# Optimization experiments

Measured on AMD Instinct MI355X. Metric: run time of the kernel, lower is better.

Reference implementation:

```python
import jax, jax.numpy as jnp
import numpy as np

DIM = 128
HEADS = 8
DK = DIM // HEADS
HID = DIM * 4
# torch: scores / math.sqrt(scale) with scale = 1/dim**0.5  ->  multiply by dim**0.25
INV = float(1.0 / np.sqrt(1.0 / np.sqrt(DIM)))


def _ln(x, g, b, eps=1e-5):
    m = jnp.mean(x, axis=-1, keepdims=True)
    v = jnp.mean((x - m) ** 2, axis=-1, keepdims=True)
    return (x - m) / jnp.sqrt(v + eps) * g + b


def _lin(x, w, b):  # torch Linear: x @ W.T + b, W:[out,in]
    return jnp.einsum('...i,oi->...o', x, w) + b


def _attention_new(node, edge, w, bv):
    # node [b,n,c], edge [b,n,n,c]; raw torch .view => row-major reshape
    b, n, c = node.shape
    q = _lin(node, w[0], bv[0]).reshape(b, HEADS, n, DK)
    k = _lin(edge, w[1], bv[1]).reshape(b, HEADS, n, n, DK)
    v = _lin(node, w[2], bv[2]).reshape(b, HEADS, n, DK)
    s = jnp.einsum('bhmd,bhmnd->bhmn', q, k) * INV
    out_attn = jax.nn.softmax(s, axis=-1)
    in_attn = jax.nn.softmax(jnp.swapaxes(s, -1, -2), axis=-1)
    eye = jnp.eye(n, dtype=s.dtype)
    # out_attn + in_attn - diag_embed(diagonal(out_attn))
    message = out_attn + in_attn - eye * out_attn
    node_h = jnp.einsum('bhmn,bhnd->bhmd', message, v).reshape(b, n, c)
    edge_h = jnp.einsum('bhmn,bhand->bhamd', message, k).reshape(b, n, n, c)
    return _lin(node_h, w[4], bv[4]), _lin(edge_h, w[3], bv[3]), message


def _enc_dec_attention(mx, px, ma, pa, w, bv):
    b, n, c = mx.shape
    P = px.shape[1]
    qx = _lin(mx, w[0], bv[0]).reshape(b, HEADS, n, DK)
    kx = _lin(px, w[1], bv[1]).reshape(b, HEADS, P, DK)
    vx = _lin(mx, w[2], bv[2]).reshape(b, HEADS, n, DK)
    qa = _lin(ma, w[3], bv[3]).reshape(b, HEADS, n, n, DK)
    ka = _lin(pa, w[4], bv[4]).reshape(b, HEADS, P, P, DK)
    va = _lin(ma, w[5], bv[5]).reshape(b, HEADS, n, n, DK)
    s = jnp.einsum('bhmd,bhnd->bhmn', qx, kx) * INV  # [b,h,n,P]
    out_attn = jax.nn.softmax(s, axis=-1)
    in_attn = jax.nn.softmax(jnp.swapaxes(s, -1, -2), axis=-1)
    message = out_attn + jnp.swapaxes(in_attn, -1, -2)
    # einsum 'bhmn,bhmd->bhmd': sum over n, elementwise scale of v
    node_h = jnp.sum(message, axis=-1)[..., None] * vx
    # 'bhmnd,bhkjd->bhmn': contract d after summing key over (k,j)
    ksum = jnp.sum(ka, axis=(2, 3))  # [b,h,d]
    se = jnp.einsum('bhmnd,bhd->bhmn', qa, ksum) * INV
    oa = jax.nn.softmax(se, axis=-1)
    ia = jax.nn.softmax(jnp.swapaxes(se, -1, -2), axis=-1)
    me = oa + jnp.swapaxes(ia, -1, -2)
    # 'bhmn,bhmkd->bhmnd': contract k
    edge_h = me[..., None] * jnp.sum(va, axis=3)[:, :, :, None, :]
    node_h = _lin(node_h.reshape(b, n, c), w[6], bv[6])
    edge_h = _lin(edge_h.reshape(b, n, n, c), w[7], bv[7])
    return edge_h, node_h, message


def _mlp(x, w1, b1, w2, b2):
    return _lin(jax.nn.sigmoid(_lin(x, w1, b1)), w2, b2)


def _decoder_block(mol_annot, prot_annot, mol_adj, prot_adj,
                   att_w, att_b, dec_w, dec_b,
                   mlp_w1, mlp_b1, mlp_w2, mlp_b2, ln_g, ln_b):
    mx = _ln(mol_annot, ln_g[2], ln_b[2])
    px = _ln(prot_annot, ln_g[3], ln_b[3])
    ma = _ln(mol_adj, ln_g[0], ln_b[0])
    pa = _ln(prot_adj, ln_g[1], ln_b[1])
    px1, pa1, _ = _attention_new(px, pa, att_w, att_b)
    px1 = _ln(px + px1, ln_g[5], ln_b[5])
    pa1 = _ln(pa + pa1, ln_g[4], ln_b[4])
    ma1, mx1, attn_dec = _enc_dec_attention(mx, px1, ma, pa1, dec_w, dec_b)
    ma1 = _ln(ma + ma1, ln_g[6], ln_b[6])
    mx1 = _ln(mx + mx1, ln_g[7], ln_b[7])
    ma2 = _mlp(ma1, mlp_w1[0], mlp_b1[0], mlp_w2[0], mlp_b2[0]) + ma1
    mx2 = _mlp(mx1, mlp_w1[1], mlp_b1[1], mlp_w2[1], mlp_b2[1]) + mx1
    edge_hidden = _ln(ma2, ln_g[8], ln_b[8])
    node_hidden = _ln(mx2, ln_g[9], ln_b[9])
    return edge_hidden, node_hidden, attn_dec


def setup_inputs() -> dict:
    key = jax.random.key(0)
    ks = jax.random.split(key, 16)
    B, N, P = 8, 64, 256
    inp = {
        'mol_annot': jax.random.normal(ks[0], (B, N, DIM), jnp.float32),
        'prot_annot': jax.random.normal(ks[1], (B, P, DIM), jnp.float32),
        'mol_adj': jax.random.normal(ks[2], (B, N, N, DIM), jnp.float32),
        'prot_adj': jax.random.normal(ks[3], (B, P, P, DIM), jnp.float32),
        # Attention_new linears: [q,k,v,out_e,out_n]
        'att_w': jax.random.normal(ks[4], (5, DIM, DIM), jnp.float32) * 0.02,
        'att_b': jax.random.normal(ks[5], (5, DIM), jnp.float32) * 0.02,
        # enc_dec linears: [q_mx,k_px,v_mx,q_ma,k_pa,v_ma,out_mx,out_ma]
        'dec_w': jax.random.normal(ks[6], (8, DIM, DIM), jnp.float32) * 0.02,
        'dec_b': jax.random.normal(ks[7], (8, DIM), jnp.float32) * 0.02,
        # MLPs: index 0 = mlp_ma, 1 = mlp_mx
        'mlp_w1': jax.random.normal(ks[8], (2, HID, DIM), jnp.float32) * 0.02,
        'mlp_b1': jax.random.normal(ks[9], (2, HID), jnp.float32) * 0.02,
        'mlp_w2': jax.random.normal(ks[10], (2, DIM, HID), jnp.float32) * 0.02,
        'mlp_b2': jax.random.normal(ks[11], (2, DIM), jnp.float32) * 0.02,
        # LayerNorms: [ln1_ma,ln1_pa,ln1_mx,ln1_px,ln2_pa,ln2_px,ln3_ma,ln3_mx,ln4_ma,ln4_mx]
        'ln_g': jnp.ones((10, DIM), jnp.float32),
        'ln_b': jnp.zeros((10, DIM), jnp.float32),
    }
    return inp


def reference(mol_annot, prot_annot, mol_adj, prot_adj, att_w, att_b,
              dec_w, dec_b, mlp_w1, mlp_b1, mlp_w2, mlp_b2, ln_g, ln_b):
    return _decoder_block(mol_annot, prot_annot, mol_adj, prot_adj,
                          att_w, att_b, dec_w, dec_b,
                          mlp_w1, mlp_b1, mlp_w2, mlp_b2, ln_g, ln_b)
```

## Files before the change

kernel.cpp:

```cpp
#include <hip/hip_runtime.h>
#include <hip/hip_bf16.h>
#include <math.h>

#define INV_SCALE 3.3635856610148585f

typedef float f32x4 __attribute__((ext_vector_type(4)));
typedef short bf16x8 __attribute__((ext_vector_type(8)));
typedef unsigned short u16;
#define MFMA(a_, b_, c_) __builtin_amdgcn_mfma_f32_16x16x32_bf16(a_, b_, c_, 0, 0, 0)

constexpr int WT_ATT = 0;
constexpr int WT_DEC = 81920;
constexpr int WT_M1  = 212992;
constexpr int WT_M2  = 344064;
constexpr int O_PX   = 475136;
constexpr int O_MX   = 737280;
constexpr int O_MA   = 802816;
constexpr int O_QL   = 4997120;
constexpr int O_VL   = 5259264;
constexpr int O_QXL  = 5521408;
constexpr int O_VXL  = 5586944;
constexpr int O_KXL  = 5652480;
constexpr int O_PX1  = 5914624;
constexpr int O_MX1  = 6176768;
constexpr int O_S    = 6242304;
constexpr int O_MSG  = 10469376;
constexpr int O_NH   = 14663680;
constexpr int O_RS   = 14925824;
constexpr int O_KS   = 14934016;
constexpr int O_SE   = 14935040;
constexpr int O_ME2  = 15197184;
constexpr int O_VAS  = 15459328;
constexpr int O_MROW = 15524864;
constexpr int O_S2   = 15528960;
constexpr int O_MA1  = 16577536;

constexpr int OUT1_OFF = 4194304;
constexpr int OUT2_OFF = 4259840;

__device__ __forceinline__ float waveSum(float v) {
#pragma unroll
  for (int o = 32; o > 0; o >>= 1) v += __shfl_down(v, o, 64);
  return v;
}

__device__ __forceinline__ void split1(float a, u16& h, u16& l) {
  unsigned ua = __float_as_uint(a) & 0xffff0000u;
  h = (u16)(ua >> 16);
  float al = a - __uint_as_float(ua);
  l = (u16)(__float_as_uint(al) >> 16);
}
__device__ __forceinline__ void split8(const float* p, bf16x8& hi, bf16x8& lo) {
#pragma unroll
  for (int i = 0; i < 8; i++) {
    float a = p[i];
    unsigned ua = __float_as_uint(a) & 0xffff0000u;
    float al = a - __uint_as_float(ua);
    hi[i] = (short)(u16)(ua >> 16);
    lo[i] = (short)(u16)(__float_as_uint(al) >> 16);
  }
}
__device__ __forceinline__ u16 rne1(float a) {
  unsigned u = __float_as_uint(a);
  u += 0x7fffu + ((u >> 16) & 1u);
  return (u16)(u >> 16);
}
__device__ __forceinline__ bf16x8 rne8(const float* p) {
  bf16x8 h;
#pragma unroll
  for (int i = 0; i < 8; i++) h[i] = (short)rne1(p[i]);
  return h;
}

__global__ __launch_bounds__(256) void prep_wt(
    const float* __restrict__ att_w, const float* __restrict__ dec_w,
    const float* __restrict__ mlp_w1, const float* __restrict__ mlp_w2,
    float* __restrict__ ws) {
  int seg = blockIdx.x, t = threadIdx.x;
  if (seg < 5) {
    const float* w = att_w + seg * 16384;
    if (seg == 1 || seg == 3) {
      u16* oh = (u16*)(ws + WT_ATT + seg * 16384);
      for (int idx = t; idx < 16384; idx += 256) {
        int e = idx & 7, lane = (idx >> 3) & 63, kk = (idx >> 9) & 3, q = idx >> 11;
        int o = q * 16 + (lane & 15), i = kk * 32 + (lane >> 4) * 8 + e;
        u16 hh, ll; split1(w[o * 128 + i], hh, ll);
        oh[idx] = hh; oh[16384 + idx] = ll;
      }
    } else {
      float* o = ws + WT_ATT + seg * 16384;
      for (int idx = t; idx < 16384; idx += 256) o[idx] = w[(idx & 127) * 128 + (idx >> 7)];
    }
  } else if (seg < 13) {
    int k = seg - 5;
    const float* w = dec_w + k * 16384;
    float* o = ws + WT_DEC + k * 16384;
    for (int idx = t; idx < 16384; idx += 256) o[idx] = w[(idx & 127) * 128 + (idx >> 7)];
  } else if (seg < 15) {
    int k = seg - 13;
    const float* w = mlp_w1 + k * 65536;
    u16* oh = (u16*)(ws + WT_M1 + k * 65536);
    for (int idx = t; idx < 65536; idx += 256) {
      int e = idx & 7, lane = (idx >> 3) & 63, kk = (idx >> 9) & 3, q = idx >> 11;
      int o = q * 16 + (lane & 15), i = kk * 32 + (lane >> 4) * 8 + e;
      oh[idx] = rne1(w[o * 128 + i]); oh[65536 + idx] = 0;
    }
  } else {
    int k = seg - 15;
    const float* w = mlp_w2 + k * 65536;
    u16* oh = (u16*)(ws + WT_M2 + k * 65536);
    for (int idx = t; idx < 65536; idx += 256) {
      int e = idx & 7, lane = (idx >> 3) & 63, kk = (idx >> 9) & 15, q = idx >> 13;
      int o = q * 16 + (lane & 15), i = kk * 32 + (lane >> 4) * 8 + e;
      oh[idx] = rne1(w[o * 512 + i]); oh[65536 + idx] = 0;
    }
  }
}

__global__ __launch_bounds__(128) void ln_rows4(const float* __restrict__ in, float* __restrict__ out,
                                                const float* __restrict__ g, const float* __restrict__ b) {
  int t = threadIdx.x;
  size_t row = (size_t)blockIdx.x * 4 + (t >> 5);
  int c4 = (t & 31) * 4;
  float4 x = *(const float4*)&in[row * 128 + c4];
  float s = x.x + x.y + x.z + x.w;
#pragma unroll
  for (int o = 16; o > 0; o >>= 1) s += __shfl_xor(s, o, 64);
  float mean = s * (1.f / 128.f);
  float dx = x.x - mean, dy = x.y - mean, dz = x.z - mean, dw = x.w - mean;
  float v = dx * dx + dy * dy + dz * dz + dw * dw;
#pragma unroll
  for (int o = 16; o > 0; o >>= 1) v += __shfl_xor(v, o, 64);
  float rstd = rsqrtf(v * (1.f / 128.f) + 1e-5f);
  float4 gv = *(const float4*)&g[c4];
  float4 bv = *(const float4*)&b[c4];
  float4 o4;
  o4.x = dx * rstd * gv.x + bv.x;
  o4.y = dy * rstd * gv.y + bv.y;
  o4.z = dz * rstd * gv.z + bv.z;
  o4.w = dw * rstd * gv.w + bv.w;
  *(float4*)&out[row * 128 + c4] = o4;
}

__global__ __launch_bounds__(128) void lin_rows2(const float* __restrict__ in,
                                                 float* __restrict__ out1, const float* __restrict__ WT1,
                                                 const float* __restrict__ b1v,
                                                 float* __restrict__ out2, const float* __restrict__ WT2,
                                                 const float* __restrict__ b2v) {
  int row = blockIdx.x, t = threadIdx.x;
  __shared__ float rl[128];
  rl[t] = in[(size_t)row * 128 + t];
  __syncthreads();
  float a1 = b1v[t], a2 = b2v[t];
#pragma unroll 8
  for (int i = 0; i < 128; i++) {
    float rv = rl[i];
    a1 += rv * WT1[i * 128 + t];
    a2 += rv * WT2[i * 128 + t];
  }
  out1[(size_t)row * 128 + t] = a1;
  out2[(size_t)row * 128 + t] = a2;
}

__global__ __launch_bounds__(128) void lin_rows(const float* __restrict__ in, float* __restrict__ out,
                                                const float* __restrict__ WT, const float* __restrict__ bias) {
  int row = blockIdx.x, t = threadIdx.x;
  __shared__ float rl[128];
  rl[t] = in[(size_t)row * 128 + t];
  __syncthreads();
  float acc = bias[t];
#pragma unroll 8
  for (int i = 0; i < 128; i++) acc += rl[i] * WT[i * 128 + t];
  out[(size_t)row * 128 + t] = acc;
}

__device__ __forceinline__ void ln32_stats(float (*tile)[132], float* psum, float* meanL, float* rstdL,
                                           int t) {
  int r = t >> 3, seg = t & 7;
  float p = 0;
#pragma unroll
  for (int k = 0; k < 16; k++) p += tile[r][seg * 16 + k];
  psum[r * 8 + seg] = p;
  __syncthreads();
  if (t < 32) { float sm = 0; for (int k = 0; k < 8; k++) sm += psum[t * 8 + k]; meanL[t] = sm * (1.f / 128.f); }
  __syncthreads();
  float mu = meanL[r];
  p = 0;
#pragma unroll
  for (int k = 0; k < 16; k++) { float d = tile[r][seg * 16 + k] - mu; p += d * d; }
  psum[r * 8 + seg] = p;
  __syncthreads();
  if (t < 32) { float sm = 0; for (int k = 0; k < 8; k++) sm += psum[t * 8 + k]; rstdL[t] = rsqrtf(sm * (1.f / 128.f) + 1e-5f); }
  __syncthreads();
}

__device__ __forceinline__ void ln64_stats(float (*tile)[132], float* psum, float* meanL, float* rstdL,
                                           int t) {
  int r = t >> 3, seg = t & 7;
  float p = 0;
#pragma unroll
  for (int k = 0; k < 16; k++) p += tile[r][seg * 16 + k];
  psum[r * 8 + seg] = p;
  __syncthreads();
  if (t < 64) { float sm = 0; for (int k = 0; k < 8; k++) sm += psum[t * 8 + k]; meanL[t] = sm * (1.f / 128.f); }
  __syncthreads();
  float mu = meanL[r];
  p = 0;
#pragma unroll
  for (int k = 0; k < 16; k++) { float d = tile[r][seg * 16 + k] - mu; p += d * d; }
  psum[r * 8 + seg] = p;
  __syncthreads();
  if (t < 64) { float sm = 0; for (int k = 0; k < 8; k++) sm += psum[t * 8 + k]; rstdL[t] = rsqrtf(sm * (1.f / 128.f) + 1e-5f); }
  __syncthreads();
}

__global__ __launch_bounds__(256, 8) void k1_fold(
    const float* __restrict__ prot_adj, const float* __restrict__ q_lin,
    const float* __restrict__ wk_orig,
    const float* __restrict__ bk,
    const float* __restrict__ g1, const float* __restrict__ b1,
    float* __restrict__ sdst) {
  __shared__ __align__(16) float paF[32][132];
  __shared__ float wq[8][132];
  __shared__ float qL[16];
  __shared__ float psum[256];
  __shared__ float meanL[32], rstdL[32];
  int t = threadIdx.x, bid = blockIdx.x;
  int b = bid >> 11, h = (bid >> 8) & 7, ai = bid & 255;
  int irow = h * 32 + (ai >> 3), j0 = (ai & 7) * 32;
  int mq = (ai >> 3) * 8 + (ai & 7);
  size_t pabase = (((size_t)(b * 256) + irow) * 256 + j0) * 128;
  {
    const float4* src4 = (const float4*)(prot_adj + pabase);
    for (int idx = t; idx < 1024; idx += 256)
      *(float4*)&paF[idx >> 5][(idx & 31) * 4] = src4[idx];
  }
  if (t < 16) qL[t] = q_lin[((size_t)(b * 256) + h * 32 + (mq >> 3)) * 128 + (mq & 7) * 16 + t];
  __syncthreads();
#pragma unroll
  for (int k = 0; k < 4; k++) {
    int o = t + k * 256;
    int g8 = o >> 7, c = o & 127;
    float s = 0;
#pragma unroll
    for (int d = 0; d < 16; d++) s += qL[d] * wk_orig[(g8 * 16 + d) * 128 + c];
    wq[g8][c] = s;
  }
  ln32_stats(paF, psum, meanL, rstdL, t);
  for (int idx = t; idx < 4096; idx += 256) {
    int r = idx >> 7, c = idx & 127;
    paF[r][c] = (paF[r][c] - meanL[r]) * rstdL[r] * g1[c] + b1[c];
  }
  __syncthreads();
  int r = t >> 3, g8 = t & 7;
  float acc = 0;
#pragma unroll
  for (int d = 0; d < 16; d++) acc += qL[d] * bk[g8 * 16 + d];
#pragma unroll 8
  for (int c = 0; c < 128; c++) acc += paF[r][c] * wq[g8][c];
  size_t sb = ((size_t)((b * 8 + h) * 256 + mq)) * 256;
  sdst[sb + t] = INV_SCALE * acc;
}

__global__ __launch_bounds__(256) void col_part(const float* __restrict__ s, float* __restrict__ pmax,
                                                float* __restrict__ psumv) {
  int bid = blockIdx.x, t = threadIdx.x;
  int bh = bid >> 3, ch = bid & 7;
  const float* sp = s + ((size_t)(bh * 256) + ch * 32) * 256 + t;
  float rm = -3.4e38f, rs = 0.f;
  for (int r = 0; r < 32; r++) {
    float x = sp[(size_t)r * 256];
    float nm = fmaxf(rm, x);
    rs = rs * __expf(rm - nm) + __expf(x - nm);
    rm = nm;
  }
  pmax[(bh * 8 + ch) * 256 + t] = rm;
  psumv[(bh * 8 + ch) * 256 + t] = rs;
}

__global__ __launch_bounds__(256, 1) void msg_tiles(const float* __restrict__ s,
                                                    const float* __restrict__ pmax, const float* __restrict__ psumv,
                                                    const float* __restrict__ v_lin,
                                                    u16* __restrict__ mhi, u16* __restrict__ mlo,
                                                    float* __restrict__ nh) {
  __shared__ __align__(16) float rowT[32][260];
  __shared__ float sT[256][33];
  __shared__ __align__(16) u16 vTh[16][264];
  __shared__ __align__(16) u16 vTl[16][264];
  __shared__ float red[256];
  __shared__ float rmax[32], rsinv[32], cmaxL[32], csinvL[32];
  int bid = blockIdx.x, t = threadIdx.x;
  int bh = bid >> 3, m0 = (bid & 7) * 32;
  int b = bh >> 3, h = bh & 7;
  size_t sbase = (size_t)(bh * 256) * 256;
  for (int idx = t; idx < 2048; idx += 256) {
    int r = idx >> 6, c4 = (idx & 63) * 4;
    *(float4*)&rowT[r][c4] = *(const float4*)&s[sbase + (size_t)(m0 + r) * 256 + c4];
  }
  for (int idx = t; idx < 2048; idx += 256) {
    int n = idx >> 3, mc4 = (idx & 7) * 4;
    float4 v4 = *(const float4*)&s[sbase + (size_t)n * 256 + m0 + mc4];
    sT[n][mc4] = v4.x; sT[n][mc4 + 1] = v4.y; sT[n][mc4 + 2] = v4.z; sT[n][mc4 + 3] = v4.w;
  }
  {
    const float4* vb4 = (const float4*)(v_lin + ((size_t)(b * 256) + h * 32) * 128);
    for (int idx = t; idx < 1024; idx += 256) {
      float4 v4 = vb4[idx];
#pragma unroll
      for (int i = 0; i < 4; i++) {
        int flat = idx * 4 + i;
        int d = flat & 15, n = flat >> 4;
        u16 hh2, ll2; split1(((const float*)&v4)[i], hh2, ll2);
        vTh[d][n] = hh2; vTl[d][n] = ll2;
      }
    }
  }
  __syncthreads();
  {
    int r = t >> 3, sg = t & 7;
    float pm = -3.4e38f;
    for (int k = 0; k < 32; k++) pm = fmaxf(pm, rowT[r][sg * 32 + k]);
    red[t] = pm;
    __syncthreads();
    if (t < 32) { float mm = red[t * 8]; for (int k = 1; k < 8; k++) mm = fmaxf(mm, red[t * 8 + k]); rmax[t] = mm; }
    __syncthreads();
    float mm = rmax[r], ps = 0;
    for (int k = 0; k < 32; k++) ps += __expf(rowT[r][sg * 32 + k] - mm);
    red[t] = ps;
    __syncthreads();
    if (t < 32) { float sm = 0; for (int k = 0; k < 8; k++) sm += red[t * 8 + k]; rsinv[t] = 1.f / sm; }
    if (t >= 64 && t < 96) {
      int mc = t - 64, col = m0 + mc;
      float cm = -3.4e38f;
      for (int c2 = 0; c2 < 8; c2++) cm = fmaxf(cm, pmax[(bh * 8 + c2) * 256 + col]);
      float cs = 0;
      for (int c2 = 0; c2 < 8; c2++) cs += psumv[(bh * 8 + c2) * 256 + col] * __expf(pmax[(bh * 8 + c2) * 256 + col] - cm);
      cmaxL[mc] = cm; csinvL[mc] = 1.f / cs;
    }
    __syncthreads();
  }
  for (int idx = t; idx < 8192; idx += 256) {
    int r = idx >> 8, n = idx & 255;
    float x = rowT[r][n];
    float outv = __expf(x - rmax[r]) * rsinv[r];
    float inval = __expf(sT[n][r] - cmaxL[r]) * csinvL[r];
    rowT[r][n] = (n == m0 + r) ? inval : (outv + inval);
  }
  __syncthreads();
  for (int fi = t; fi < 1024; fi += 256) {
    int r = fi >> 5, fc = fi & 31;
    int m = m0 + r;
    int lane = (fc & 3) * 16 + (m & 15);
    size_t base = (size_t)bh * 65536 + (size_t)(m >> 4) * 4096 + (size_t)(fc >> 2) * 512 + lane * 8;
    bf16x8 h8, l8;
    split8(&rowT[r][fc * 8], h8, l8);
    *(bf16x8*)&mhi[base] = h8;
    *(bf16x8*)&mlo[base] = l8;
  }
  int w = t >> 6, l = t & 63, lr = l & 15, lk = l >> 4;
  if (w < 2) {
    f32x4 acc = (f32x4){0.f, 0.f, 0.f, 0.f};
#pragma unroll
    for (int kk = 0; kk < 8; kk++) {
      bf16x8 ah, al;
      split8(&rowT[w * 16 + lr][kk * 32 + lk * 8], ah, al);
      bf16x8 bhv = *(const bf16x8*)&vTh[lr][kk * 32 + lk * 8];
      bf16x8 blv = *(const bf16x8*)&vTl[lr][kk * 32 + lk * 8];
      acc = MFMA(ah, bhv, acc);
      acc = MFMA(al, bhv, acc);
      acc = MFMA(ah, blv, acc);
    }
#pragma unroll
    for (int j = 0; j < 4; j++)
      nh[((size_t)(bh * 256) + m0 + w * 16 + lk * 4 + j) * 16 + lr] = acc[j];
  }
}

__global__ __launch_bounds__(128) void px1_kernel(const float* __restrict__ px, const float* __restrict__ nh,
                                                  const float* __restrict__ WT, const float* __restrict__ bias,
                                                  const float* __restrict__ g, const float* __restrict__ bt,
                                                  float* __restrict__ px1) {
  int p = blockIdx.x, t = threadIdx.x;
  int b = p >> 8, pl = p & 255, h = pl >> 5;
  __shared__ float nodeL[128];
  __shared__ float scr[2];
  nodeL[t] = nh[((size_t)(b * 8 + h) * 256 + ((pl & 31) * 8 + (t >> 4))) * 16 + (t & 15)];
  __syncthreads();
  float acc = bias[t];
#pragma unroll 8
  for (int i = 0; i < 128; i++) acc += nodeL[i] * WT[i * 128 + t];
  float val = px[(size_t)p * 128 + t] + acc;
  float v = waveSum(val);
  if ((t & 63) == 0) scr[t >> 6] = v;
  __syncthreads();
  float mean = (scr[0] + scr[1]) * (1.f / 128.f);
  __syncthreads();
  float dd = val - mean;
  v = waveSum(dd * dd);
  if ((t & 63) == 0) scr[t >> 6] = v;
  __syncthreads();
  float rstd = rsqrtf((scr[0] + scr[1]) * (1.f / 128.f) + 1e-5f);
  px1[(size_t)p * 128 + t] = dd * rstd * g[t] + bt[t];
}

__global__ __launch_bounds__(512, 1) void s2_fused(const float* __restrict__ qxl, const float* __restrict__ kxl,
                                                   float* __restrict__ out2, float* __restrict__ mrow) {
  __shared__ float kxL[256 * 17];
  __shared__ float qxL[64 * 17];
  __shared__ float sL[64][257];
  __shared__ float rmaxL[64], rsinv[64];
  __shared__ float cmaxL[256], csinv[256];
  int bh = blockIdx.x, t = threadIdx.x;
  int b = bh >> 3, h = bh & 7;
  for (int idx = t; idx < 4096; idx += 512) {
    int pl = idx >> 7, cc = idx & 127;
    kxL[(pl * 8 + (cc >> 4)) * 17 + (cc & 15)] = kxl[((size_t)(b * 256) + h * 32 + pl) * 128 + cc];
  }
  for (int idx = t; idx < 1024; idx += 512) {
    int rl = idx >> 7, cc = idx & 127;
    qxL[(rl * 8 + (cc >> 4)) * 17 + (cc & 15)] = qxl[((size_t)(b * 64) + h * 8 + rl) * 128 + cc];
  }
  __syncthreads();
  {
    int p = t & 255, mh = t >> 8;
    float kr[16];
#pragma unroll
    for (int d = 0; d < 16; d++) kr[d] = kxL[p * 17 + d];
    for (int m = mh * 32; m < mh * 32 + 32; m++) {
      float dot = 0;
#pragma unroll
      for (int d = 0; d < 16; d++) dot += qxL[m * 17 + d] * kr[d];
      sL[m][p] = INV_SCALE * dot;
    }
  }
  __syncthreads();
  if (t < 64) {
    float mx = -3.4e38f;
    for (int p = 0; p < 256; p++) mx = fmaxf(mx, sL[t][p]);
    float sm = 0;
    for (int p = 0; p < 256; p++) sm += __expf(sL[t][p] - mx);
    rmaxL[t] = mx; rsinv[t] = 1.f / sm;
  }
  if (t < 256) {
    float mx = -3.4e38f;
    for (int m = 0; m < 64; m++) mx = fmaxf(mx, sL[m][t]);
    float sm = 0;
    for (int m = 0; m < 64; m++) sm += __expf(sL[m][t] - mx);
    cmaxL[t] = mx; csinv[t] = 1.f / sm;
  }
  __syncthreads();
  for (int idx = t; idx < 16384; idx += 512) {
    int m = idx >> 8, p = idx & 255;
    float x = sL[m][p];
    float val = __expf(x - rmaxL[m]) * rsinv[m] + __expf(x - cmaxL[p]) * csinv[p];
    out2[(size_t)bh * 16384 + idx] = val;
    sL[m][p] = val;
  }
  __syncthreads();
  if (t < 64) {
    float sm = 0;
    for (int p = 0; p < 256; p++) sm += sL[t][p];
    mrow[bh * 64 + t] = sm;
  }
}

__global__ __launch_bounds__(128) void mx1_kernel(const float* __restrict__ mx, const float* __restrict__ mrow,
                                                  const float* __restrict__ vxl, const float* __restrict__ WT,
                                                  const float* __restrict__ bias, const float* __restrict__ g,
                                                  const float* __restrict__ bt, float* __restrict__ mx1) {
  int rg = blockIdx.x, t = threadIdx.x;
  int b = rg >> 6, rl = rg & 63, h = rl >> 3;
  __shared__ float nodeL[128];
  __shared__ float scr[2];
  int m = (rl & 7) * 8 + (t >> 4);
  float vxv = vxl[((size_t)(b * 64) + h * 8 + (m >> 3)) * 128 + (m & 7) * 16 + (t & 15)];
  nodeL[t] = mrow[(b * 8 + h) * 64 + m] * vxv;
  __syncthreads();
  float acc = bias[t];
#pragma unroll 8
  for (int i = 0; i < 128; i++) acc += nodeL[i] * WT[i * 128 + t];
  float val = mx[(size_t)rg * 128 + t] + acc;
  float v = waveSum(val);
  if ((t & 63) == 0) scr[t >> 6] = v;
  __syncthreads();
  float mean = (scr[0] + scr[1]) * (1.f / 128.f);
  __syncthreads();
  float dd = val - mean;
  v = waveSum(dd * dd);
  if ((t & 63) == 0) scr[t >> 6] = v;
  __syncthreads();
  float rstd = rsqrtf((scr[0] + scr[1]) * (1.f / 128.f) + 1e-5f);
  mx1[(size_t)rg * 128 + t] = dd * rstd * g[t] + bt[t];
}

__global__ __launch_bounds__(512, 4) void k5_row(
    const float* __restrict__ prot_adj,
    const u16* __restrict__ msg_hi, const u16* __restrict__ msg_lo,
    const u16* __restrict__ wk_hi,
    const u16* __restrict__ wo_hi,
    const float* __restrict__ bk, const float* __restrict__ bo,
    const float* __restrict__ g1, const float* __restrict__ b1,
    const float* __restrict__ g4, const float* __restrict__ b4,
    float* __restrict__ rs128) {
  __shared__ __align__(16) unsigned char Lmem[72704];
  float (*paF)[132] = (float(*)[132])Lmem;
  u16* kBh = (u16*)(Lmem + 33792);
  u16* kBl = (u16*)(Lmem + 33792 + 16896);
  float (*e2)[132] = (float(*)[132])(Lmem + 33792);
  float* psum  = (float*)(Lmem + 67584);
  float* meanL = (float*)(Lmem + 69632);
  float* rstdL = (float*)(Lmem + 69888);
  float* accL  = (float*)(Lmem + 70144);
  float* scr2  = (float*)(Lmem + 70656);
  int t = threadIdx.x;
  int bid = (blockIdx.x & 7) * 256 + (blockIdx.x >> 3);
  int b = bid >> 8, h = (bid >> 5) & 7, irow_rel = bid & 31;
  int irow = h * 32 + irow_rel;
  int w = t >> 6, l = t & 63;
  const int lr = l & 15, lk = l >> 4;
  const int wr = w & 3, wq = w >> 2;
  const size_t mb = ((size_t)(b * 8 + h)) << 16;
  if (t < 128) accL[t] = 0.f;
  for (int chunk = 0; chunk < 4; chunk++) {
    __syncthreads();
    {
      size_t pabase = (((size_t)(b * 256) + irow) * 256 + chunk * 64) * 128;
      const float4* src4 = (const float4*)(prot_adj + pabase);
      for (int idx = t; idx < 2048; idx += 512)
        *(float4*)&paF[idx >> 5][(idx & 31) * 4] = src4[idx];
    }
    __syncthreads();
    ln64_stats(paF, psum, meanL, rstdL, t);
    for (int idx = t; idx < 8192; idx += 512) {
      int r = idx >> 7, c = idx & 127;
      paF[r][c] = (paF[r][c] - meanL[r]) * rstdL[r] * g1[c] + b1[c];
    }
    __syncthreads();
    {
      f32x4 acc1[4];
#pragma unroll
      for (int qq = 0; qq < 4; qq++) acc1[qq] = (f32x4){0.f, 0.f, 0.f, 0.f};
#pragma unroll 1
      for (int kk = 0; kk < 4; kk++) {
        bf16x8 ah, al;
        split8(&paF[wr * 16 + lr][kk * 32 + lk * 8], ah, al);
#pragma unroll
        for (int qq = 0; qq < 4; qq++) {
          int q = wq * 4 + qq;
          bf16x8 bh = *(const bf16x8*)&wk_hi[q * 2048 + kk * 512 + l * 8];
          bf16x8 bl = *(const bf16x8*)&wk_hi[16384 + q * 2048 + kk * 512 + l * 8];
          acc1[qq] = MFMA(ah, bh, acc1[qq]);
          acc1[qq] = MFMA(al, bh, acc1[qq]);
          acc1[qq] = MFMA(ah, bl, acc1[qq]);
        }
      }
#pragma unroll
      for (int qq = 0; qq < 4; qq++) {
        int q = wq * 4 + qq;
        float bkv = bk[q * 16 + lr];
#pragma unroll
        for (int j = 0; j < 4; j++) {
          int rloc = wr * 16 + lk * 4 + j;
          int n = (rloc & 31) * 8 + q;
          int colB = (rloc >> 5) * 16 + lr;
          u16 hh, ll; split1(acc1[qq][j] + bkv, hh, ll);
          kBh[colB * 264 + n] = hh; kBl[colB * 264 + n] = ll;
        }
      }
    }
    __syncthreads();
    f32x4 eacc[2][2];
#pragma unroll
    for (int mt = 0; mt < 2; mt++)
#pragma unroll
      for (int ct = 0; ct < 2; ct++) eacc[mt][ct] = (f32x4){0.f, 0.f, 0.f, 0.f};
#pragma unroll 1
    for (int kk = 0; kk < 8; kk++) {
      bf16x8 bhv[2], blv[2];
#pragma unroll
      for (int ct = 0; ct < 2; ct++) {
        bhv[ct] = *(const bf16x8*)&kBh[(ct * 16 + lr) * 264 + kk * 32 + lk * 8];
        blv[ct] = *(const bf16x8*)&kBl[(ct * 16 + lr) * 264 + kk * 32 + lk * 8];
      }
#pragma unroll
      for (int mt = 0; mt < 2; mt++) {
        size_t ro = mb + (size_t)((w * 2 + mt) * 4096 + kk * 512 + l * 8);
        bf16x8 ah = *(const bf16x8*)&msg_hi[ro];
        bf16x8 al = *(const bf16x8*)&msg_lo[ro];
#pragma unroll
        for (int ct = 0; ct < 2; ct++) {
          eacc[mt][ct] = MFMA(ah, bhv[ct], eacc[mt][ct]);
          eacc[mt][ct] = MFMA(al, bhv[ct], eacc[mt][ct]);
          eacc[mt][ct] = MFMA(ah, blv[ct], eacc[mt][ct]);
        }
      }
    }
    __syncthreads();
#pragma unroll
    for (int mt = 0; mt < 2; mt++)
#pragma unroll
      for (int ct = 0; ct < 2; ct++)
#pragma unroll
        for (int j = 0; j < 4; j++) {
          int m = w * 32 + mt * 16 + lk * 4 + j;
          int colE = ct * 16 + lr;
          e2[(colE >> 4) * 32 + (m >> 3)][(m & 7) * 16 + (colE & 15)] = eacc[mt][ct][j];
        }
    __syncthreads();
    {
      f32x4 oacc[4];
#pragma unroll
      for (int qq = 0; qq < 4; qq++) oacc[qq] = (f32x4){0.f, 0.f, 0.f, 0.f};
#pragma unroll 1
      for (int kk = 0; kk < 4; kk++) {
        bf16x8 ah, al;
        split8(&e2[wr * 16 + lr][kk * 32 + lk * 8], ah, al);
#pragma unroll
        for (int qq = 0; qq < 4; qq++) {
          int q = wq * 4 + qq;
          bf16x8 bh = *(const bf16x8*)&wo_hi[q * 2048 + kk * 512 + l * 8];
          bf16x8 bl = *(const bf16x8*)&wo_hi[16384 + q * 2048 + kk * 512 + l * 8];
          oacc[qq] = MFMA(ah, bh, oacc[qq]);
          oacc[qq] = MFMA(al, bh, oacc[qq]);
          oacc[qq] = MFMA(ah, bl, oacc[qq]);
        }
      }
      __syncthreads();
#pragma unroll
      for (int qq = 0; qq < 4; qq++) {
        int o = (wq * 4 + qq) * 16 + lr;
        float bv = bo[o];
#pragma unroll
        for (int j = 0; j < 4; j++) {
          int rloc = wr * 16 + lk * 4 + j;
          paF[rloc][o] = oacc[qq][j] + bv + paF[rloc][o];
        }
      }
    }
    __syncthreads();
    ln64_stats(paF, psum, meanL, rstdL, t);
    {
      int c = t & 127, rh = t >> 7;
      float part = 0;
#pragma unroll
      for (int rr = 0; rr < 16; rr++) {
        int r2 = rh * 16 + rr;
        part += (paF[r2][c] - meanL[r2]) * rstdL[r2];
      }
      scr2[rh * 128 + c] = part;
    }
    __syncthreads();
    if (t < 128) accL[t] += scr2[t] + scr2[128 + t] + scr2[256 + t] + scr2[384 + t];
  }
  __syncthreads();
  if (t < 128)
    atomicAdd(&rs128[(b * 8 + h) * 128 + t], g4[t] * accL[t] + 256.f * b4[t]);
}

__global__ __launch_bounds__(128) void ksum_kernel(const float* __restrict__ rs128, const float* __restrict__ WT,
                                                   const float* __restrict__ bias, float* __restrict__ ks) {
  int bh = blockIdx.x, t = threadIdx.x;
  __shared__ float rsL[128];
  __shared__ float pcL[128];
  rsL[t] = rs128[bh * 128 + t];
  __syncthreads();
  float pc = 0;
#pragma unroll 8
  for (int i = 0; i < 128; i++) pc += rsL[i] * WT[i * 128 + t];
  pcL[t] = pc;
  __syncthreads();
  if (t < 16) {
    float kv = 0;
    for (int g8 = 0; g8 < 8; g8++) kv += pcL[g8 * 16 + t] + 8192.f * bias[g8 * 16 + t];
    ks[bh * 16 + t] = kv;
  }
}

__global__ __launch_bounds__(256) void se_vasum(
    const float* __restrict__ ma, const float* __restrict__ WTqa, const float* __restrict__ bqa,
    const float* __restrict__ WTva, const float* __restrict__ bva,
    const float* __restrict__ ks, float* __restrict__ se, float* __restrict__ vas) {
  __shared__ __align__(16) float w[16384];
  __shared__ float rows[16 * 129];
  __shared__ float red[4096];
  int t = threadIdx.x, bid = blockIdx.x;
  int b = bid >> 8, iq = (bid >> 2) & 63, jb = bid & 3, j0 = jb * 16;
  int h = iq >> 3;
  float ksumv[16];
#pragma unroll
  for (int d = 0; d < 16; d++) ksumv[d] = ks[(b * 8 + h) * 16 + d];
  size_t rowbase = ((size_t)(b * 64 + iq) * 64 + j0) * 128;
  for (int idx = t; idx < 2048; idx += 256) rows[(idx >> 7) * 129 + (idx & 127)] = ma[rowbase + idx];
  for (int idx = t; idx < 16384; idx += 256) w[idx] = WTqa[idx];
  __syncthreads();
  int g8 = t >> 5, r = (t >> 1) & 15, iseg = t & 1;
  {
    float acc[16];
#pragma unroll
    for (int d = 0; d < 16; d++) acc[d] = 0.f;
    for (int ii = 0; ii < 64; ii++) {
      int i2 = iseg * 64 + ii;
      float pav = rows[r * 129 + i2];
      float wv[16];
      const float4* w4 = (const float4*)&w[i2 * 128 + g8 * 16];
      *(float4*)&wv[0] = w4[0]; *(float4*)&wv[4] = w4[1]; *(float4*)&wv[8] = w4[2]; *(float4*)&wv[12] = w4[3];
#pragma unroll
      for (int d = 0; d < 16; d++) acc[d] += pav * wv[d];
    }
    float sval = 0;
#pragma unroll
    for (int d = 0; d < 16; d++) sval += acc[d] * ksumv[d];
    red[(r * 8 + g8) * 2 + iseg] = sval;
    __syncthreads();
    if (t < 128) {
      int rr = t >> 3, gg = t & 7;
      float sv = red[(rr * 8 + gg) * 2] + red[(rr * 8 + gg) * 2 + 1];
      float bdot = 0;
#pragma unroll
      for (int d = 0; d < 16; d++) bdot += bqa[gg * 16 + d] * ksumv[d];
      sv += bdot;
      int jj = j0 + rr;
      int mm = (iq & 7) * 8 + (jj >> 3);
      int n2 = (jj & 7) * 8 + gg;
      se[((size_t)(b * 8 + h) * 64 + mm) * 64 + n2] = INV_SCALE * sv;
    }
    __syncthreads();
  }
  for (int idx = t; idx < 16384; idx += 256) w[idx] = WTva[idx];
  __syncthreads();
  {
    float acc[16];
#pragma unroll
    for (int d = 0; d < 16; d++) acc[d] = 0.f;
    for (int ii = 0; ii < 64; ii++) {
      int i2 = iseg * 64 + ii;
      float pav = rows[r * 129 + i2];
      float wv[16];
      const float4* w4 = (const float4*)&w[i2 * 128 + g8 * 16];
      *(float4*)&wv[0] = w4[0]; *(float4*)&wv[4] = w4[1]; *(float4*)&wv[8] = w4[2]; *(float4*)&wv[12] = w4[3];
#pragma unroll
      for (int d = 0; d < 16; d++) acc[d] += pav * wv[d];
    }
    if (iseg == 0) {
#pragma unroll
      for (int d = 0; d < 16; d++) acc[d] += bva[g8 * 16 + d];
    }
#pragma unroll
    for (int d = 0; d < 16; d++) red[t * 16 + d] = acc[d];
    __syncthreads();
    if (t < 32) {
      int mgrp = t >> 4, d = t & 15;
      float sm = 0;
      for (int gg = 0; gg < 8; gg++)
        for (int rr = mgrp * 8; rr < mgrp * 8 + 8; rr++) {
          sm += red[(gg * 32 + rr * 2) * 16 + d] + red[(gg * 32 + rr * 2 + 1) * 16 + d];
        }
      int mv = (iq & 7) * 8 + jb * 2 + mgrp;
      atomicAdd(&vas[((size_t)(b * 8 + h) * 64 + mv) * 16 + d], sm);
    }
  }
}

__global__ __launch_bounds__(256) void me2_kernel(const float* __restrict__ se, float* __restrict__ me2) {
  __shared__ float sL[64 * 65];
  __shared__ float rmaxL[64], rsinv[64], cmaxL[64], csinv[64];
  int bh = blockIdx.x, t = threadIdx.x;
  for (int idx = t; idx < 4096; idx += 256) sL[(idx >> 6) * 65 + (idx & 63)] = se[(size_t)bh * 4096 + idx];
  __syncthreads();
  if (t < 64) {
    float mx = -3.4e38f;
    for (int n = 0; n < 64; n++) mx = fmaxf(mx, sL[t * 65 + n]);
    float sm = 0;
    for (int n = 0; n < 64; n++) sm += __expf(sL[t * 65 + n] - mx);
    rmaxL[t] = mx; rsinv[t] = 1.f / sm;
  } else if (t < 128) {
    int n = t - 64;
    float mx = -3.4e38f;
    for (int m = 0; m < 64; m++) mx = fmaxf(mx, sL[m * 65 + n]);
    float sm = 0;
    for (int m = 0; m < 64; m++) sm += __expf(sL[m * 65 + n] - mx);
    cmaxL[n] = mx; csinv[n] = 1.f / sm;
  }
  __syncthreads();
  for (int idx = t; idx < 4096; idx += 256) {
    int m = idx >> 6, n = idx & 63;
    float x = sL[m * 65 + n];
    me2[(size_t)bh * 4096 + idx] = __expf(x - rmaxL[m]) * rsinv[m] + __expf(x - cmaxL[n]) * csinv[n];
  }
}

__global__ __launch_bounds__(256) void ma1_kernel(
    const float* __restrict__ ma, const float* __restrict__ me2, const float* __restrict__ vas,
    const float* __restrict__ WT, const float* __restrict__ bias,
    const float* __restrict__ g, const float* __restrict__ bt, float* __restrict__ ma1) {
  __shared__ __align__(16) float w[16384];
  __shared__ float rows[16 * 129];
  __shared__ float ored[4096];
  __shared__ float psum[256];
  __shared__ float meanL[16], rstdL[16];
// ... 48 lines not shown
#pragma unroll
    for (int k = 0; k < 8; k++) { float d = rows[rr * 129 + seg * 8 + k] - mu; p += d * d; }
    psum[rr * 16 + seg] = p;
    __syncthreads();
    if (t < 16) { float sm = 0; for (int k = 0; k < 16; k++) sm += psum[t * 16 + k]; rstdL[t] = rsqrtf(sm * (1.f / 128.f) + 1e-5f); }
    __syncthreads();
  }
  for (int idx = t; idx < 2048; idx += 256) {
    int r2 = idx >> 7, c = idx & 127;
    ma1[rowbase + idx] = (rows[r2 * 129 + c] - meanL[r2]) * rstdL[r2] * g[c] + bt[c];
  }
}

__global__ __launch_bounds__(256, 4) void mlp_mfma(
    const float* __restrict__ in,
    const u16* __restrict__ w1h,
    const float* __restrict__ b1,
    const u16* __restrict__ w2h,
    const float* __restrict__ b2,
    const float* __restrict__ g, const float* __restrict__ bt, float* __restrict__ out) {
  __shared__ __align__(16) float rowL[16][132];
  __shared__ __align__(16) u16 hh[16][520];
  __shared__ float psum[256];
  __shared__ float meanL[16], rstdL[16];
  int t = threadIdx.x, bid = blockIdx.x;
  int w = t >> 6, l = t & 63, lr = l & 15, lk = l >> 4;
  size_t base = (size_t)bid * 2048;
  {
    const float4* src4 = (const float4*)(in + base);
    for (int idx = t; idx < 512; idx += 256)
      *(float4*)&rowL[idx >> 5][(idx & 31) * 4] = src4[idx];
  }
  __syncthreads();
  {
    f32x4 acc1[8];
#pragma unroll
    for (int nt = 0; nt < 8; nt++) acc1[nt] = (f32x4){0.f, 0.f, 0.f, 0.f};
#pragma unroll 1
    for (int kk = 0; kk < 4; kk++) {
      bf16x8 ah = rne8(&rowL[lr][kk * 32 + lk * 8]);
#pragma unroll
      for (int nt = 0; nt < 8; nt++) {
        int q = w * 8 + nt;
        bf16x8 bh = *(const bf16x8*)&w1h[q * 2048 + kk * 512 + l * 8];
        acc1[nt] = MFMA(ah, bh, acc1[nt]);
      }
    }
#pragma unroll
    for (int nt = 0; nt < 8; nt++) {
      int o = w * 128 + nt * 16 + lr;
      float bb = b1[o];
#pragma unroll
      for (int j = 0; j < 4; j++) {
        int m = lk * 4 + j;
        float hv = 1.f / (1.f + __expf(-(acc1[nt][j] + bb)));
        hh[m][o] = rne1(hv);
      }
    }
  }
  __syncthreads();
  {
    f32x4 acc2[2];
#pragma unroll
    for (int nt = 0; nt < 2; nt++) acc2[nt] = (f32x4){0.f, 0.f, 0.f, 0.f};
#pragma unroll 1
    for (int kk = 0; kk < 16; kk++) {
      bf16x8 ah = *(const bf16x8*)&hh[lr][kk * 32 + lk * 8];
#pragma unroll
      for (int nt = 0; nt < 2; nt++) {
        int q = w * 2 + nt;
        bf16x8 bh = *(const bf16x8*)&w2h[q * 8192 + kk * 512 + l * 8];
        acc2[nt] = MFMA(ah, bh, acc2[nt]);
      }
    }
    __syncthreads();
#pragma unroll
    for (int nt = 0; nt < 2; nt++) {
      int c = w * 32 + nt * 16 + lr;
      float bb = b2[c];
#pragma unroll
      for (int j = 0; j < 4; j++) {
        int m = lk * 4 + j;
        rowL[m][c] = acc2[nt][j] + bb + rowL[m][c];
      }
    }
  }
  __syncthreads();
  {
    int rr = t >> 4, seg = t & 15;
    float p = 0;
#pragma unroll
    for (int k = 0; k < 8; k++) p += rowL[rr][seg * 8 + k];
    psum[rr * 16 + seg] = p;
    __syncthreads();
    if (t < 16) { float sm = 0; for (int k = 0; k < 16; k++) sm += psum[t * 16 + k]; meanL[t] = sm * (1.f / 128.f); }
    __syncthreads();
    float mu = meanL[rr];
    p = 0;
#pragma unroll
    for (int k = 0; k < 8; k++) { float d = rowL[rr][seg * 8 + k] - mu; p += d * d; }
    psum[rr * 16 + seg] = p;
    __syncthreads();
    if (t < 16) { float sm = 0; for (int k = 0; k < 16; k++) sm += psum[t * 16 + k]; rstdL[t] = rsqrtf(sm * (1.f / 128.f) + 1e-5f); }
    __syncthreads();
  }
  for (int idx = t; idx < 2048; idx += 256) {
    int r2 = idx >> 7, cc = idx & 127;
    out[base + idx] = (rowL[r2][cc] - meanL[r2]) * rstdL[r2] * g[cc] + bt[cc];
  }
}

extern "C" void kernel_launch(void* const* d_in, const int* in_sizes, int n_in,
                              void* d_out, int out_size, void* d_ws, size_t ws_size,
                              hipStream_t stream) {
  (void)in_sizes; (void)n_in; (void)out_size; (void)ws_size;
  const float* mol_annot  = (const float*)d_in[0];
  const float* prot_annot = (const float*)d_in[1];
  const float* mol_adj    = (const float*)d_in[2];
  const float* prot_adj   = (const float*)d_in[3];
  const float* att_w = (const float*)d_in[4];
  const float* att_b = (const float*)d_in[5];
  const float* dec_w = (const float*)d_in[6];
  const float* dec_b = (const float*)d_in[7];
  const float* mlp_w1 = (const float*)d_in[8];
  const float* mlp_b1 = (const float*)d_in[9];
  const float* mlp_w2 = (const float*)d_in[10];
  const float* mlp_b2 = (const float*)d_in[11];
  const float* ln_g = (const float*)d_in[12];
  const float* ln_b = (const float*)d_in[13];
  float* out = (float*)d_out;
  float* ws = (float*)d_ws;

  const u16* wk_hi = (const u16*)(ws + WT_ATT + 16384);
  const u16* wo_hi = (const u16*)(ws + WT_ATT + 3 * 16384);
  u16* msg_hi = (u16*)(ws + O_MA1);
  u16* msg_lo = msg_hi + 4194304;
  float* pmaxp = ws + O_MSG;
  float* psump = ws + O_MSG + 131072;

  hipMemsetAsync(ws + O_RS, 0, 8192 * sizeof(float), stream);
  hipMemsetAsync(ws + O_VAS, 0, 65536 * sizeof(float), stream);
  prep_wt<<<17, 256, 0, stream>>>(att_w, dec_w, mlp_w1, mlp_w2, ws);
  ln_rows4<<<512, 128, 0, stream>>>(prot_annot, ws + O_PX, ln_g + 384, ln_b + 384);
  ln_rows4<<<128, 128, 0, stream>>>(mol_annot, ws + O_MX, ln_g + 256, ln_b + 256);
  ln_rows4<<<8192, 128, 0, stream>>>(mol_adj, ws + O_MA, ln_g, ln_b);
  lin_rows2<<<2048, 128, 0, stream>>>(ws + O_PX, ws + O_QL, ws + WT_ATT, att_b,
                                      ws + O_VL, ws + WT_ATT + 2 * 16384, att_b + 256);
  lin_rows2<<<512, 128, 0, stream>>>(ws + O_MX, ws + O_QXL, ws + WT_DEC, dec_b,
                                     ws + O_VXL, ws + WT_DEC + 2 * 16384, dec_b + 256);
  k1_fold<<<16384, 256, 0, stream>>>(prot_adj, ws + O_QL, att_w + 16384, att_b + 128,
                                     ln_g + 128, ln_b + 128, ws + O_S);
  col_part<<<512, 256, 0, stream>>>(ws + O_S, pmaxp, psump);
  msg_tiles<<<512, 256, 0, stream>>>(ws + O_S, pmaxp, psump, ws + O_VL, msg_hi, msg_lo, ws + O_NH);
  px1_kernel<<<2048, 128, 0, stream>>>(ws + O_PX, ws + O_NH, ws + WT_ATT + 4 * 16384, att_b + 512,
                                       ln_g + 640, ln_b + 640, ws + O_PX1);
  lin_rows<<<2048, 128, 0, stream>>>(ws + O_PX1, ws + O_KXL, ws + WT_DEC + 16384, dec_b + 128);
  s2_fused<<<64, 512, 0, stream>>>(ws + O_QXL, ws + O_KXL, out + OUT2_OFF, ws + O_MROW);
  mx1_kernel<<<512, 128, 0, stream>>>(ws + O_MX, ws + O_MROW, ws + O_VXL, ws + WT_DEC + 6 * 16384,
                                      dec_b + 768, ln_g + 896, ln_b + 896, ws + O_MX1);
  k5_row<<<2048, 512, 0, stream>>>(prot_adj, msg_hi, msg_lo, wk_hi, wo_hi,
                                   att_b + 128, att_b + 384,
                                   ln_g + 128, ln_b + 128, ln_g + 512, ln_b + 512, ws + O_RS);
  ksum_kernel<<<64, 128, 0, stream>>>(ws + O_RS, ws + WT_DEC + 4 * 16384, dec_b + 512, ws + O_KS);
  se_vasum<<<2048, 256, 0, stream>>>(ws + O_MA, ws + WT_DEC + 3 * 16384, dec_b + 384,
                                     ws + WT_DEC + 5 * 16384, dec_b + 640, ws + O_KS, ws + O_SE, ws + O_VAS);
  me2_kernel<<<64, 256, 0, stream>>>(ws + O_SE, ws + O_ME2);
  ma1_kernel<<<2048, 256, 0, stream>>>(ws + O_MA, ws + O_ME2, ws + O_VAS, ws + WT_DEC + 7 * 16384,
                                       dec_b + 896, ln_g + 768, ln_b + 768, ws + O_MA1);
  mlp_mfma<<<2048, 256, 0, stream>>>(ws + O_MA1, (const u16*)(ws + WT_M1), mlp_b1,
                                     (const u16*)(ws + WT_M2), mlp_b2,
                                     ln_g + 1024, ln_b + 1024, out);
  mlp_mfma<<<32, 256, 0, stream>>>(ws + O_MX1, (const u16*)(ws + WT_M1 + 65536), mlp_b1 + 512,
                                   (const u16*)(ws + WT_M2 + 65536), mlp_b2 + 128,
                                   ln_g + 1152, ln_b + 1152, out + OUT1_OFF);
}
```

Measured before the change: 841.6 us.

## Halve k5_row chunk size to shrink LDS and fuse px1 with kx linear

Measured after the change: 910.6 us. 8.2% more time.

```diff
diff --git a/kernel.cpp b/kernel.cpp
--- a/kernel.cpp
+++ b/kernel.cpp
@@ -162,18 +162,6 @@
   out2[(size_t)row * 128 + t] = a2;
 }
 
-__global__ __launch_bounds__(128) void lin_rows(const float* __restrict__ in, float* __restrict__ out,
-                                                const float* __restrict__ WT, const float* __restrict__ bias) {
-  int row = blockIdx.x, t = threadIdx.x;
-  __shared__ float rl[128];
-  rl[t] = in[(size_t)row * 128 + t];
-  __syncthreads();
-  float acc = bias[t];
-#pragma unroll 8
-  for (int i = 0; i < 128; i++) acc += rl[i] * WT[i * 128 + t];
-  out[(size_t)row * 128 + t] = acc;
-}
-
 __device__ __forceinline__ void ln32_stats(float (*tile)[132], float* psum, float* meanL, float* rstdL,
                                            int t) {
   int r = t >> 3, seg = t & 7;
@@ -194,23 +182,23 @@
   __syncthreads();
 }
 
-__device__ __forceinline__ void ln64_stats(float (*tile)[132], float* psum, float* meanL, float* rstdL,
-                                           int t) {
-  int r = t >> 3, seg = t & 7;
+__device__ __forceinline__ void ln32b_stats(float (*tile)[132], float* psum, float* meanL, float* rstdL,
+                                            int t) {
+  int r = t >> 4, seg = t & 15;
   float p = 0;
 #pragma unroll
-  for (int k = 0; k < 16; k++) p += tile[r][seg * 16 + k];
-  psum[r * 8 + seg] = p;
-  __syncthreads();
-  if (t < 64) { float sm = 0; for (int k = 0; k < 8; k++) sm += psum[t * 8 + k]; meanL[t] = sm * (1.f / 128.f); }
+  for (int k = 0; k < 8; k++) p += tile[r][seg * 8 + k];
+  psum[r * 16 + seg] = p;
+  __syncthreads();
+  if (t < 32) { float sm = 0; for (int k = 0; k < 16; k++) sm += psum[t * 16 + k]; meanL[t] = sm * (1.f / 128.f); }
   __syncthreads();
   float mu = meanL[r];
   p = 0;
 #pragma unroll
-  for (int k = 0; k < 16; k++) { float d = tile[r][seg * 16 + k] - mu; p += d * d; }
-  psum[r * 8 + seg] = p;
-  __syncthreads();
-  if (t < 64) { float sm = 0; for (int k = 0; k < 8; k++) sm += psum[t * 8 + k]; rstdL[t] = rsqrtf(sm * (1.f / 128.f) + 1e-5f); }
+  for (int k = 0; k < 8; k++) { float d = tile[r][seg * 8 + k] - mu; p += d * d; }
+  psum[r * 16 + seg] = p;
+  __syncthreads();
+  if (t < 32) { float sm = 0; for (int k = 0; k < 16; k++) sm += psum[t * 16 + k]; rstdL[t] = rsqrtf(sm * (1.f / 128.f) + 1e-5f); }
   __syncthreads();
 }
 
@@ -376,19 +364,21 @@
   }
 }
 
-__global__ __launch_bounds__(128) void px1_kernel(const float* __restrict__ px, const float* __restrict__ nh,
-                                                  const float* __restrict__ WT, const float* __restrict__ bias,
-                                                  const float* __restrict__ g, const float* __restrict__ bt,
-                                                  float* __restrict__ px1) {
+__global__ __launch_bounds__(128) void px1k_kernel(const float* __restrict__ px, const float* __restrict__ nh,
+                                                   const float* __restrict__ WTo, const float* __restrict__ bo,
+                                                   const float* __restrict__ g, const float* __restrict__ bt,
+                                                   const float* __restrict__ WTk, const float* __restrict__ bkx,
+                                                   float* __restrict__ kxl) {
   int p = blockIdx.x, t = threadIdx.x;
   int b = p >> 8, pl = p & 255, h = pl >> 5;
   __shared__ float nodeL[128];
+  __shared__ float px1L[128];
   __shared__ float scr[2];
   nodeL[t] = nh[((size_t)(b * 8 + h) * 256 + ((pl & 31) * 8 + (t >> 4))) * 16 + (t & 15)];
   __syncthreads();
-  float acc = bias[t];
+  float acc = bo[t];
 #pragma unroll 8
-  for (int i = 0; i < 128; i++) acc += nodeL[i] * WT[i * 128 + t];
+  for (int i = 0; i < 128; i++) acc += nodeL[i] * WTo[i * 128 + t];
   float val = px[(size_t)p * 128 + t] + acc;
   float v = waveSum(val);
   if ((t & 63) == 0) scr[t >> 6] = v;
@@ -400,7 +390,12 @@
   if ((t & 63) == 0) scr[t >> 6] = v;
   __syncthreads();
   float rstd = rsqrtf((scr[0] + scr[1]) * (1.f / 128.f) + 1e-5f);
-  px1[(size_t)p * 128 + t] = dd * rstd * g[t] + bt[t];
+  px1L[t] = dd * rstd * g[t] + bt[t];
+  __syncthreads();
+  float a2 = bkx[t];
+#pragma unroll 8
+  for (int i = 0; i < 128; i++) a2 += px1L[i] * WTk[i * 128 + t];
+  kxl[(size_t)p * 128 + t] = a2;
 }
 
 __global__ __launch_bounds__(512, 1) void s2_fused(const float* __restrict__ qxl, const float* __restrict__ kxl,
@@ -502,51 +497,51 @@
     const float* __restrict__ g1, const float* __restrict__ b1,
     const float* __restrict__ g4, const float* __restrict__ b4,
     float* __restrict__ rs128) {
-  __shared__ __align__(16) unsigned char Lmem[72704];
+  __shared__ __align__(16) unsigned char Lmem[38656];
   float (*paF)[132] = (float(*)[132])Lmem;
-  u16* kBh = (u16*)(Lmem + 33792);
-  u16* kBl = (u16*)(Lmem + 33792 + 16896);
-  float (*e2)[132] = (float(*)[132])(Lmem + 33792);
-  float* psum  = (float*)(Lmem + 67584);
-  float* meanL = (float*)(Lmem + 69632);
-  float* rstdL = (float*)(Lmem + 69888);
-  float* accL  = (float*)(Lmem + 70144);
-  float* scr2  = (float*)(Lmem + 70656);
+  u16* kBh = (u16*)(Lmem + 16896);
+  u16* kBl = (u16*)(Lmem + 16896 + 8448);
+  float (*e2)[132] = (float(*)[132])(Lmem + 16896);
+  float* psum  = (float*)(Lmem + 33792);
+  float* meanL = (float*)(Lmem + 35840);
+  float* rstdL = (float*)(Lmem + 35968);
+  float* accL  = (float*)(Lmem + 36096);
+  float* scr2  = (float*)(Lmem + 36608);
   int t = threadIdx.x;
   int bid = (blockIdx.x & 7) * 256 + (blockIdx.x >> 3);
   int b = bid >> 8, h = (bid >> 5) & 7, irow_rel = bid & 31;
   int irow = h * 32 + irow_rel;
   int w = t >> 6, l = t & 63;
   const int lr = l & 15, lk = l >> 4;
-  const int wr = w & 3, wq = w >> 2;
+  const int wr = w & 1, wq = w >> 1;
   const size_t mb = ((size_t)(b * 8 + h)) << 16;
   if (t < 128) accL[t] = 0.f;
-  for (int chunk = 0; chunk < 4; chunk++) {
+  for (int chunk = 0; chunk < 8; chunk++) {
     __syncthreads();
     {
-      size_t pabase = (((size_t)(b * 256) + irow) * 256 + chunk * 64) * 128;
+      size_t pabase = (((size_t)(b * 256) + irow) * 256 + chunk * 32) * 128;
       const float4* src4 = (const float4*)(prot_adj + pabase);
-      for (int idx = t; idx < 2048; idx += 512)
+      for (int idx = t; idx < 1024; idx += 512)
         *(float4*)&paF[idx >> 5][(idx & 31) * 4] = src4[idx];
     }
     __syncthreads();
-    ln64_stats(paF, psum, meanL, rstdL, t);
-    for (int idx = t; idx < 8192; idx += 512) {
+    ln32b_stats(paF, psum, meanL, rstdL, t);
+    for (int idx = t; idx < 4096; idx += 512) {
       int r = idx >> 7, c = idx & 127;
       paF[r][c] = (paF[r][c] - meanL[r]) * rstdL[r] * g1[c] + b1[c];
     }
     __syncthreads();
     {
-      f32x4 acc1[4];
-#pragma unroll
-      for (int qq = 0; qq < 4; qq++) acc1[qq] = (f32x4){0.f, 0.f, 0.f, 0.f};
+      f32x4 acc1[2];
+#pragma unroll
+      for (int qq = 0; qq < 2; qq++) acc1[qq] = (f32x4){0.f, 0.f, 0.f, 0.f};
 #pragma unroll 1
       for (int kk = 0; kk < 4; kk++) {
         bf16x8 ah, al;
         split8(&paF[wr * 16 + lr][kk * 32 + lk * 8], ah, al);
 #pragma unroll
-        for (int qq = 0; qq < 4; qq++) {
-          int q = wq * 4 + qq;
+        for (int qq = 0; qq < 2; qq++) {
+          int q = wq * 2 + qq;
           bf16x8 bh = *(const bf16x8*)&wk_hi[q * 2048 + kk * 512 + l * 8];
           bf16x8 bl = *(const bf16x8*)&wk_hi[16384 + q * 2048 + kk * 512 + l * 8];
           acc1[qq] = MFMA(ah, bh, acc1[qq]);
@@ -555,69 +550,56 @@
         }
       }
 #pragma unroll
-      for (int qq = 0; qq < 4; qq++) {
-        int q = wq * 4 + qq;
+      for (int qq = 0; qq < 2; qq++) {
+        int q = wq * 2 + qq;
         float bkv = bk[q * 16 + lr];
 #pragma unroll
         for (int j = 0; j < 4; j++) {
           int rloc = wr * 16 + lk * 4 + j;
-          int n = (rloc & 31) * 8 + q;
-          int colB = (rloc >> 5) * 16 + lr;
+          int n = rloc * 8 + q;
           u16 hh, ll; split1(acc1[qq][j] + bkv, hh, ll);
-          kBh[colB * 264 + n] = hh; kBl[colB * 264 + n] = ll;
+          kBh[lr * 264 + n] = hh; kBl[lr * 264 + n] = ll;
         }
       }
     }
     __syncthreads();
-    f32x4 eacc[2][2];
-#pragma unroll
-    for (int mt = 0; mt < 2; mt++)
-#pragma unroll
-      for (int ct = 0; ct < 2; ct++) eacc[mt][ct] = (f32x4){0.f, 0.f, 0.f, 0.f};
+    f32x4 eacc[2];
+#pragma unroll
+    for (int mt = 0; mt < 2; mt++) eacc[mt] = (f32x4){0.f, 0.f, 0.f, 0.f};
 #pragma unroll 1
     for (int kk = 0; kk < 8; kk++) {
-      bf16x8 bhv[2], blv[2];
-#pragma unroll
-      for (int ct = 0; ct < 2; ct++) {
-        bhv[ct] = *(const bf16x8*)&kBh[(ct * 16 + lr) * 264 + kk * 32 + lk * 8];
-        blv[ct] = *(const bf16x8*)&kBl[(ct * 16 + lr) * 264 + kk * 32 + lk * 8];
-      }
+      bf16x8 bhv = *(const bf16x8*)&kBh[lr * 264 + kk * 32 + lk * 8];
+      bf16x8 blv = *(const bf16x8*)&kBl[lr * 264 + kk * 32 + lk * 8];
 #pragma unroll
       for (int mt = 0; mt < 2; mt++) {
         size_t ro = mb + (size_t)((w * 2 + mt) * 4096 + kk * 512 + l * 8);
         bf16x8 ah = *(const bf16x8*)&msg_hi[ro];
         bf16x8 al = *(const bf16x8*)&msg_lo[ro];
-#pragma unroll
-        for (int ct = 0; ct < 2; ct++) {
-          eacc[mt][ct] = MFMA(ah, bhv[ct], eacc[mt][ct]);
-          eacc[mt][ct] = MFMA(al, bhv[ct], eacc[mt][ct]);
-          eacc[mt][ct] = MFMA(ah, blv[ct], eacc[mt][ct]);
-        }
+        eacc[mt] = MFMA(ah, bhv, eacc[mt]);
+        eacc[mt] = MFMA(al, bhv, eacc[mt]);
+        eacc[mt] = MFMA(ah, blv, eacc[mt]);
       }
     }
     __syncthreads();
 #pragma unroll
     for (int mt = 0; mt < 2; mt++)
 #pragma unroll
-      for (int ct = 0; ct < 2; ct++)
-#pragma unroll
-        for (int j = 0; j < 4; j++) {
-          int m = w * 32 + mt * 16 + lk * 4 + j;
-          int colE = ct * 16 + lr;
-          e2[(colE >> 4) * 32 + (m >> 3)][(m & 7) * 16 + (colE & 15)] = eacc[mt][ct][j];
-        }
+      for (int j = 0; j < 4; j++) {
+        int m = w * 32 + mt * 16 + lk * 4 + j;
+        e2[m >> 3][(m & 7) * 16 + lr] = eacc[mt][j];
+      }
     __syncthreads();
     {
-      f32x4 oacc[4];
-#pragma unroll
-      for (int qq = 0; qq < 4; qq++) oacc[qq] = (f32x4){0.f, 0.f, 0.f, 0.f};
+      f32x4 oacc[2];
+#pragma unroll
+      for (int qq = 0; qq < 2; qq++) oacc[qq] = (f32x4){0.f, 0.f, 0.f, 0.f};
 #pragma unroll 1
       for (int kk = 0; kk < 4; kk++) {
         bf16x8 ah, al;
         split8(&e2[wr * 16 + lr][kk * 32 + lk * 8], ah, al);
 #pragma unroll
-        for (int qq = 0; qq < 4; qq++) {
-          int q = wq * 4 + qq;
+        for (int qq = 0; qq < 2; qq++) {
+          int q = wq * 2 + qq;
           bf16x8 bh = *(const bf16x8*)&wo_hi[q * 2048 + kk * 512 + l * 8];
           bf16x8 bl = *(const bf16x8*)&wo_hi[16384 + q * 2048 + kk * 512 + l * 8];
           oacc[qq] = MFMA(ah, bh, oacc[qq]);
@@ -627,8 +609,8 @@
       }
       __syncthreads();
 #pragma unroll
-      for (int qq = 0; qq < 4; qq++) {
-        int o = (wq * 4 + qq) * 16 + lr;
+      for (int qq = 0; qq < 2; qq++) {
+        int o = (wq * 2 + qq) * 16 + lr;
         float bv = bo[o];
 #pragma unroll
         for (int j = 0; j < 4; j++) {
@@ -638,13 +620,13 @@
       }
     }
     __syncthreads();
-    ln64_stats(paF, psum, meanL, rstdL, t);
+    ln32b_stats(paF, psum, meanL, rstdL, t);
     {
       int c = t & 127, rh = t >> 7;
       float part = 0;
 #pragma unroll
-      for (int rr = 0; rr < 16; rr++) {
-        int r2 = rh * 16 + rr;
+      for (int rr = 0; rr < 8; rr++) {
+        int r2 = rh * 8 + rr;
         part += (paF[r2][c] - meanL[r2]) * rstdL[r2];
       }
       scr2[rh * 128 + c] = part;
@@ -999,9 +981,9 @@
                                      ln_g + 128, ln_b + 128, ws + O_S);
   col_part<<<512, 256, 0, stream>>>(ws + O_S, pmaxp, psump);
   msg_tiles<<<512, 256, 0, stream>>>(ws + O_S, pmaxp, psump, ws + O_VL, msg_hi, msg_lo, ws + O_NH);
-  px1_kernel<<<2048, 128, 0, stream>>>(ws + O_PX, ws + O_NH, ws + WT_ATT + 4 * 16384, att_b + 512,
-                                       ln_g + 640, ln_b + 640, ws + O_PX1);
-  lin_rows<<<2048, 128, 0, stream>>>(ws + O_PX1, ws + O_KXL, ws + WT_DEC + 16384, dec_b + 128);
+  px1k_kernel<<<2048, 128, 0, stream>>>(ws + O_PX, ws + O_NH, ws + WT_ATT + 4 * 16384, att_b + 512,
+                                        ln_g + 640, ln_b + 640, ws + WT_DEC + 16384, dec_b + 128,
+                                        ws + O_KXL);
   s2_fused<<<64, 512, 0, stream>>>(ws + O_QXL, ws + O_KXL, out + OUT2_OFF, ws + O_MROW);
   mx1_kernel<<<512, 128, 0, stream>>>(ws + O_MX, ws + O_MROW, ws + O_VXL, ws + WT_DEC + 6 * 16384,
                                       dec_b + 768, ln_g + 896, ln_b + 896, ws + O_MX1);
```
